# Kernel tuning notes

Measured on AMD Instinct MI355X. Metric: run time of the kernel, lower is better.

The kernel has to match this reference:

```python
import jax, jax.numpy as jnp
import numpy as np


def setup_inputs() -> dict:
    key = jax.random.key(0)
    ks = jax.random.split(key, 8)
    B, C, T, V = 64, 256, 64, 25
    h = 8
    x_cls = jax.random.normal(ks[0], (B, C, 1, V), dtype=jnp.float32)
    x_patch = jax.random.normal(ks[1], (B, C, T, V), dtype=jnp.float32)
    s = 0.02
    q_w = jax.random.normal(ks[2], (C, C), dtype=jnp.float32) * s
    k_w = jax.random.normal(ks[3], (C, C), dtype=jnp.float32) * s
    v_w = jax.random.normal(ks[4], (C, C), dtype=jnp.float32) * s
    temp = jnp.ones((h, 1), dtype=jnp.float32)
    proj_w = jax.random.normal(ks[5], (C, C), dtype=jnp.float32) * s
    proj_b = jnp.zeros((C,), dtype=jnp.float32)
    return {"x_cls": x_cls, "x_patch": x_patch, "q_w": q_w, "k_w": k_w,
            "v_w": v_w, "temp": temp, "proj_w": proj_w, "proj_b": proj_b}


def reference(x_cls, x_patch, q_w, k_w, v_w, temp, proj_w, proj_b):
    B, C, _, V = x_cls.shape
    T = x_patch.shape[2]
    h = temp.shape[0]
    hd = C // h
    # (B, C, 1, V) -> (B, V, C) token layout; patches -> (B, T*V, C)
    xc = jnp.transpose(x_cls.reshape(B, C, V), (0, 2, 1))
    xp = jnp.transpose(x_patch.reshape(B, C, T * V), (0, 2, 1))
    # nn.Linear: y = x @ W.T (no bias since qkv_bias=False)
    q = (xc @ q_w.T).reshape(B, V, h, hd).transpose(0, 2, 1, 3)        # (B,h,V,hd)
    k = (xp @ k_w.T).reshape(B, T * V, h, hd).transpose(0, 2, 1, 3)    # (B,h,TV,hd)
    v = (xp @ v_w.T).reshape(B, T * V, h, hd).transpose(0, 2, 1, 3)    # (B,h,TV,hd)
    # scores: (B,h,V,TV), scaled by 1/sqrt(hd) then per-head temperature
    scale = 1.0 / jnp.sqrt(jnp.asarray(hd, dtype=q.dtype))
    attn = jnp.einsum('bhqd,bhkd->bhqk', q, k) * scale
    attn = attn * temp[None, :, :, None]  # temp (h,1) -> broadcast (1,h,1,1)
    attn = jax.nn.softmax(attn, axis=-1)
    out = jnp.einsum('bhqk,bhkd->bhqd', attn, v)                       # (B,h,V,hd)
    out = out.transpose(0, 2, 1, 3).reshape(B, V, C)
    out = out @ proj_w.T + proj_b
    return jnp.transpose(out, (0, 2, 1)).reshape(B, C, 1, V)
```

## Files before the change

### kernel.cpp

```cpp
#include <hip/hip_runtime.h>

#define B_ 64
#define C_ 256
#define TV_ 1600
#define V_ 25
#define H_ 8

typedef __attribute__((ext_vector_type(2))) int   intx2;
typedef __attribute__((ext_vector_type(4))) int   intx4;
typedef __attribute__((ext_vector_type(4))) float floatx4;
typedef __attribute__((ext_vector_type(8))) short short8;

__device__ __forceinline__ unsigned short f2bf(float f) {
    union { float f; unsigned u; } c; c.f = f;
    unsigned u = c.u;
    u += 0x7fffu + ((u >> 16) & 1u);
    return (unsigned short)(u >> 16);
}
__device__ __forceinline__ float bf2f(unsigned short s) {
    union { unsigned u; float f; } c; c.u = ((unsigned)s) << 16;
    return c.f;
}
__device__ __forceinline__ int pk_bf2(float a, float b) {
    return (int)((unsigned)f2bf(a) | ((unsigned)f2bf(b) << 16));
}

__global__ __launch_bounds__(256) void kz_zero(float* __restrict__ zbase,
        const float* __restrict__ vw, const float* __restrict__ pw,
        unsigned short* __restrict__ VWB, unsigned short* __restrict__ PWB) {
    const int blk = blockIdx.x;
    if (blk < 528) {
        const int i = blk * 256 + threadIdx.x;
        ((floatx4*)zbase)[i] = (floatx4){0.f, 0.f, 0.f, 0.f};
    } else {
        const int g = (blk - 528) * 256 + threadIdx.x;
        const floatx4 v = ((const floatx4*)vw)[g];
        const floatx4 p = ((const floatx4*)pw)[g];
        ((intx2*)VWB)[g] = (intx2){pk_bf2(v[0], v[1]), pk_bf2(v[2], v[3])};
        ((intx2*)PWB)[g] = (intx2){pk_bf2(p[0], p[1]), pk_bf2(p[2], p[3])};
    }
}

__global__ __launch_bounds__(256) void k1_trans(const float* __restrict__ xp,
                                                unsigned short* __restrict__ XF) {
    __shared__ float xs[128 * 68];
    const int blk = blockIdx.x;
    const int b = blk / 25, nb = blk - b * 25;
    const int n0 = nb * 64;
    const int t = threadIdx.x;
    const int cl = t & 127, nh = (t >> 7) * 32;
    const int n = t & 63, cq = t >> 6;
    for (int p = 0; p < 2; p++) {
        const float* src = xp + ((size_t)(b * C_ + p * 128 + cl)) * TV_ + n0 + nh;
        floatx4 v[8];
        #pragma unroll
        for (int j = 0; j < 8; j++) v[j] = *(const floatx4*)(src + 4 * j);
        if (p) __syncthreads();
        #pragma unroll
        for (int j = 0; j < 8; j++) *(floatx4*)&xs[cl * 68 + nh + 4 * j] = v[j];
        __syncthreads();
        #pragma unroll
        for (int j4 = 0; j4 < 4; j4++) {
            const int cgl = cq * 4 + j4, c8 = cgl * 8;
            intx4 w;
            w[0] = pk_bf2(xs[(c8 + 0) * 68 + n], xs[(c8 + 1) * 68 + n]);
            w[1] = pk_bf2(xs[(c8 + 2) * 68 + n], xs[(c8 + 3) * 68 + n]);
            w[2] = pk_bf2(xs[(c8 + 4) * 68 + n], xs[(c8 + 5) * 68 + n]);
            w[3] = pk_bf2(xs[(c8 + 6) * 68 + n], xs[(c8 + 7) * 68 + n]);
            const size_t chunk = (size_t)(b * 50 + nb * 2 + (n >> 5)) * 1024
                               + (p * 16 + cgl) * 32 + (n & 31);
            *(intx4*)(XF + chunk * 8) = w;
        }
        if (!p) __syncthreads();
    }
}

__global__ __launch_bounds__(256) void k0_qtilde(const float* __restrict__ xcls,
        const float* __restrict__ qw, const float* __restrict__ kw,
        const float* __restrict__ temp, unsigned short* __restrict__ QT) {
    __shared__ float xq[25 * 260];
    __shared__ float qh[25 * 33];
    __shared__ float kws[32 * 264];
    const int blk = blockIdx.x;
    const int b = blk >> 3, h = blk & 7;
    const int t = threadIdx.x;
    {
        const float* src = xcls + ((size_t)(b * C_ + t)) * V_;
        #pragma unroll
        for (int q = 0; q < V_; q++) xq[q * 260 + t] = src[q];
    }
    {
        const int d = t >> 3, c0 = (t & 7) * 32;
        const float* src = kw + (size_t)(h * 32 + d) * C_ + c0;
        #pragma unroll
        for (int j4 = 0; j4 < 8; j4++)
            *(floatx4*)&kws[d * 264 + c0 + 4 * j4] = *(const floatx4*)(src + 4 * j4);
    }
    __syncthreads();
    for (int idx = t; idx < 800; idx += 256) {
        const int q = idx >> 5, d = idx & 31;
        const float* qwr = qw + (size_t)(h * 32 + d) * C_;
        float acc = 0.f;
        for (int c4 = 0; c4 < 64; c4++) {
            const floatx4 a = *(const floatx4*)(qwr + 4 * c4);
            const floatx4 x = *(const floatx4*)&xq[q * 260 + 4 * c4];
            acc += a[0] * x[0] + a[1] * x[1] + a[2] * x[2] + a[3] * x[3];
        }
        qh[q * 33 + d] = acc;
    }
    __syncthreads();
    const float scale = temp[h] * 0.17677669529663689f * 1.4426950408889634f;
    const int qp = t & 31, cg = t >> 5;
    const int c0 = cg * 32;
    if (qp < 25) {
        floatx4 a4[8];
        #pragma unroll
        for (int j = 0; j < 8; j++) a4[j] = (floatx4){0.f, 0.f, 0.f, 0.f};
        for (int d = 0; d < 32; d++) {
            const float a = qh[qp * 33 + d];
            #pragma unroll
            for (int j4 = 0; j4 < 8; j4++) {
                const floatx4 k4 = *(const floatx4*)&kws[d * 264 + c0 + 4 * j4];
                a4[j4][0] += a * k4[0]; a4[j4][1] += a * k4[1];
                a4[j4][2] += a * k4[2]; a4[j4][3] += a * k4[3];
            }
        }
        unsigned short* dst = QT + ((size_t)((b * H_ + h) * 25 + qp)) * C_ + c0;
        #pragma unroll
        for (int j8 = 0; j8 < 4; j8++) {
            intx4 w;
            w[0] = pk_bf2(scale * a4[j8 * 2][0],     scale * a4[j8 * 2][1]);
            w[1] = pk_bf2(scale * a4[j8 * 2][2],     scale * a4[j8 * 2][3]);
            w[2] = pk_bf2(scale * a4[j8 * 2 + 1][0], scale * a4[j8 * 2 + 1][1]);
            w[3] = pk_bf2(scale * a4[j8 * 2 + 1][2], scale * a4[j8 * 2 + 1][3]);
            *(intx4*)(dst + j8 * 8) = w;
        }
    }
}

__global__ __launch_bounds__(512, 2) void k2_attn(
        const unsigned short* __restrict__ XF, const unsigned short* __restrict__ QT,
        const unsigned short* __restrict__ VWB, float* __restrict__ OA,
        float* __restrict__ L) {
    __shared__ unsigned short Xs[8192];
    __shared__ unsigned short Ps[8][32 * 40];
    __shared__ unsigned short Vs[8][32 * 40];

    const int blk = blockIdx.x;
    const int b = blk & 63, s = blk >> 6;
    const int tid = threadIdx.x;
    const int h = tid >> 6;
    const int lane = tid & 63;
    const int quad = lane >> 4, l16 = lane & 15;

    short8 qf[2][8];
    {
        const unsigned short* qb = QT + (size_t)(b * H_ + h) * 25 * C_;
        #pragma unroll
        for (int mt = 0; mt < 2; mt++)
            #pragma unroll
            for (int ks = 0; ks < 8; ks++)
                qf[mt][ks] = *(const short8*)(qb + (mt * 16 + l16) * C_ + ks * 32 + quad * 8);
    }
    short8 vwf[2][8];
    #pragma unroll
    for (int dt = 0; dt < 2; dt++)
        #pragma unroll
        for (int ks = 0; ks < 8; ks++)
            vwf[dt][ks] = *(const short8*)(VWB + (size_t)(h * 32 + dt * 16 + l16) * C_ + ks * 32 + quad * 8);

    floatx4 oc[2][2];
    #pragma unroll
    for (int mt = 0; mt < 2; mt++)
        #pragma unroll
        for (int dt = 0; dt < 2; dt++) oc[mt][dt] = (floatx4){0.f, 0.f, 0.f, 0.f};
    float lsum[2][4];
    #pragma unroll
    for (int mt = 0; mt < 2; mt++)
        #pragma unroll
        for (int r = 0; r < 4; r++) lsum[mt][r] = 0.f;

    const unsigned short* xf_base = XF + (size_t)(b * 50 + s * 5) * 1024 * 8;
    intx4 px0 = *(const intx4*)(xf_base + (size_t)(tid * 2 + 0) * 8);
    intx4 px1 = *(const intx4*)(xf_base + (size_t)(tid * 2 + 1) * 8);

    for (int ti = 0; ti < 5; ti++) {
        *(intx4*)&Xs[(tid * 2 + 0) * 8] = px0;
        *(intx4*)&Xs[(tid * 2 + 1) * 8] = px1;
        __syncthreads();
        if (ti < 4) {
            const unsigned short* nxt = xf_base + (size_t)(ti + 1) * 1024 * 8;
            px0 = *(const intx4*)(nxt + (size_t)(tid * 2 + 0) * 8);
            px1 = *(const intx4*)(nxt + (size_t)(tid * 2 + 1) * 8);
        }
        floatx4 sc[2][2], va[2][2];
        #pragma unroll
        for (int i = 0; i < 2; i++)
            #pragma unroll
            for (int j = 0; j < 2; j++) {
                sc[i][j] = (floatx4){0.f, 0.f, 0.f, 0.f};
                va[i][j] = (floatx4){0.f, 0.f, 0.f, 0.f};
            }
        #pragma unroll
        for (int ks = 0; ks < 8; ks++) {
            const short8 xf0 = *(const short8*)&Xs[(((ks * 4 + quad) * 32) + l16) * 8];
            const short8 xf1 = *(const short8*)&Xs[(((ks * 4 + quad) * 32) + 16 + l16) * 8];
            sc[0][0] = __builtin_amdgcn_mfma_f32_16x16x32_bf16(qf[0][ks], xf0, sc[0][0], 0, 0, 0);
            sc[0][1] = __builtin_amdgcn_mfma_f32_16x16x32_bf16(qf[0][ks], xf1, sc[0][1], 0, 0, 0);
            sc[1][0] = __builtin_amdgcn_mfma_f32_16x16x32_bf16(qf[1][ks], xf0, sc[1][0], 0, 0, 0);
            sc[1][1] = __builtin_amdgcn_mfma_f32_16x16x32_bf16(qf[1][ks], xf1, sc[1][1], 0, 0, 0);
            va[0][0] = __builtin_amdgcn_mfma_f32_16x16x32_bf16(xf0, vwf[0][ks], va[0][0], 0, 0, 0);
            va[0][1] = __builtin_amdgcn_mfma_f32_16x16x32_bf16(xf0, vwf[1][ks], va[0][1], 0, 0, 0);
            va[1][0] = __builtin_amdgcn_mfma_f32_16x16x32_bf16(xf1, vwf[0][ks], va[1][0], 0, 0, 0);
            va[1][1] = __builtin_amdgcn_mfma_f32_16x16x32_bf16(xf1, vwf[1][ks], va[1][1], 0, 0, 0);
        }
        #pragma unroll
        for (int mt = 0; mt < 2; mt++)
            #pragma unroll
            for (int g = 0; g < 2; g++)
                #pragma unroll
                for (int r = 0; r < 4; r++) {
                    const float p = __builtin_amdgcn_exp2f(sc[mt][g][r]);
                    lsum[mt][r] += p;
                    Ps[h][(mt * 16 + quad * 4 + r) * 40 + g * 16 + l16] = f2bf(p);
                }
        #pragma unroll
        for (int g = 0; g < 2; g++)
            #pragma unroll
            for (int dt = 0; dt < 2; dt++)
                *(intx2*)&Vs[h][(dt * 16 + l16) * 40 + g * 16 + quad * 4] =
                    (intx2){pk_bf2(va[g][dt][0], va[g][dt][1]),
                            pk_bf2(va[g][dt][2], va[g][dt][3])};
        #pragma unroll
        for (int mt = 0; mt < 2; mt++) {
            const short8 pa = *(const short8*)&Ps[h][(mt * 16 + l16) * 40 + quad * 8];
            #pragma unroll
            for (int dt = 0; dt < 2; dt++) {
                const short8 vb = *(const short8*)&Vs[h][(dt * 16 + l16) * 40 + quad * 8];
                oc[mt][dt] = __builtin_amdgcn_mfma_f32_16x16x32_bf16(pa, vb, oc[mt][dt], 0, 0, 0);
            }
        }
        __syncthreads();
    }
    #pragma unroll
    for (int mt = 0; mt < 2; mt++)
        #pragma unroll
        for (int r = 0; r < 4; r++) {
            float v = lsum[mt][r];
            #pragma unroll
            for (int off = 1; off < 16; off <<= 1) v += __shfl_xor(v, off, 64);
            lsum[mt][r] = v;
        }
    const size_t bh = (size_t)(b * H_ + h);
    if (l16 == 0) {
        #pragma unroll
        for (int mt = 0; mt < 2; mt++)
            #pragma unroll
            for (int r = 0; r < 4; r++) {
                const int q = mt * 16 + quad * 4 + r;
                if (q < 25) atomicAdd(&L[bh * 32 + q], lsum[mt][r]);
            }
    }
    #pragma unroll
    for (int mt = 0; mt < 2; mt++)
        #pragma unroll
        for (int dt = 0; dt < 2; dt++)
            #pragma unroll
            for (int r = 0; r < 4; r++) {
                const int q = mt * 16 + quad * 4 + r;
                if (q < 25)
                    atomicAdd(&OA[bh * 1024 + q * 32 + dt * 16 + l16], oc[mt][dt][r]);
            }
}

__global__ __launch_bounds__(256) void k3_proj(const float* __restrict__ OA,
        const float* __restrict__ Lsum, const unsigned short* __restrict__ PWB,
        const float* __restrict__ pb, float* __restrict__ y) {
    __shared__ unsigned short OB[32 * 264];
    __shared__ float rl_s[256];
    const int blk = blockIdx.x;
    const int b = blk >> 1, i0 = (blk & 1) * 128;
    const int t = threadIdx.x;
    const int wv = t >> 6, lane = t & 63;
    const int quad = lane >> 4, l16 = lane & 15;
    {
        const int h = t >> 5, q = t & 31;
        const float lv = Lsum[(size_t)(b * H_ + h) * 32 + q];
        rl_s[t] = (q < 25) ? 1.0f / lv : 0.0f;
    }
    __syncthreads();
    for (int idx = t; idx < 8192; idx += 256) {
        const int q = idx >> 8, j = idx & 255;
        const int h2 = j >> 5, d = j & 31;
        const float val = (q < 25)
            ? OA[(size_t)(b * H_ + h2) * 1024 + q * 32 + d] * rl_s[h2 * 32 + q] : 0.f;
        OB[q * 264 + j] = f2bf(val);
    }
    __syncthreads();
    floatx4 oc[2][2];
    #pragma unroll
    for (int mt = 0; mt < 2; mt++)
        #pragma unroll
        for (int ntp = 0; ntp < 2; ntp++) oc[mt][ntp] = (floatx4){0.f, 0.f, 0.f, 0.f};
    #pragma unroll
    for (int ks = 0; ks < 8; ks++) {
        const short8 a0 = *(const short8*)&OB[l16 * 264 + ks * 32 + quad * 8];
        const short8 a1 = *(const short8*)&OB[(16 + l16) * 264 + ks * 32 + quad * 8];
        #pragma unroll
        for (int ntp = 0; ntp < 2; ntp++) {
            const int i = i0 + (wv * 2 + ntp) * 16 + l16;
            const short8 bv = *(const short8*)(PWB + (size_t)i * C_ + ks * 32 + quad * 8);
            oc[0][ntp] = __builtin_amdgcn_mfma_f32_16x16x32_bf16(a0, bv, oc[0][ntp], 0, 0, 0);
            oc[1][ntp] = __builtin_amdgcn_mfma_f32_16x16x32_bf16(a1, bv, oc[1][ntp], 0, 0, 0);
        }
    }
    #pragma unroll
    for (int ntp = 0; ntp < 2; ntp++) {
        const int i = i0 + (wv * 2 + ntp) * 16 + l16;
        const float bias = pb[i];
        #pragma unroll
        for (int mt = 0; mt < 2; mt++)
            #pragma unroll
            for (int r = 0; r < 4; r++) {
                const int q = mt * 16 + quad * 4 + r;
                if (q < 25) y[(size_t)b * 6400 + i * 25 + q] = oc[mt][ntp][r] + bias;
            }
    }
}

extern "C" void kernel_launch(void* const* d_in, const int* in_sizes, int n_in,
                              void* d_out, int out_size, void* d_ws, size_t ws_size,
                              hipStream_t stream) {
    const float* xcls = (const float*)d_in[0];
    const float* xp   = (const float*)d_in[1];
    const float* qw   = (const float*)d_in[2];
    const float* kw   = (const float*)d_in[3];
    const float* vw   = (const float*)d_in[4];
    const float* temp = (const float*)d_in[5];
    const float* pw   = (const float*)d_in[6];
    const float* pb   = (const float*)d_in[7];
    float* y = (float*)d_out;

    if (ws_size < (size_t)61415424) return;
    char* ws = (char*)d_ws;
    unsigned short* XF  = (unsigned short*)ws;
    unsigned short* QT  = (unsigned short*)(ws + 52428800);
    float*          OA  = (float*)(ws + 58990592);
    float*          L   = (float*)(ws + 61087744);
    unsigned short* VWB = (unsigned short*)(ws + 61153280);
    unsigned short* PWB = (unsigned short*)(ws + 61284352);

    hipLaunchKernelGGL(kz_zero,  dim3(592),  dim3(256), 0, stream, OA, vw, pw, VWB, PWB);
    hipLaunchKernelGGL(k1_trans, dim3(1600), dim3(256), 0, stream, xp, XF);
    hipLaunchKernelGGL(k0_qtilde,dim3(512),  dim3(256), 0, stream, xcls, qw, kw, temp, QT);
    hipLaunchKernelGGL(k2_attn,  dim3(640),  dim3(512), 0, stream, XF, QT, VWB, OA, L);
    hipLaunchKernelGGL(k3_proj,  dim3(128),  dim3(256), 0, stream, OA, L, PWB, pb, y);
}
```

Measured before the change: 299.6 us.

## Merge preprocessing kernels, double-buffer X tiles in attention, widen projection grid

Merges the zero/convert, transpose and q-tilde kernels into one launch that dispatches on block index, which removes two kernel launches and their serialization gaps. The q-tilde path now reads k_w straight from global memory instead of staging it in shared memory. The attention kernel double-buffers the X tile in LDS so the next tile is stored after compute, leaving one barrier per iteration. The projection kernel uses twice as many blocks, each computing half as many output columns, to raise parallelism at the cost of redundant OB staging.

Result: no change. 296.6 us (-1.0%).

```diff
diff --git a/kernel.cpp b/kernel.cpp
--- a/kernel.cpp
+++ b/kernel.cpp
@@ -25,115 +25,110 @@
     return (int)((unsigned)f2bf(a) | ((unsigned)f2bf(b) << 16));
 }
 
-__global__ __launch_bounds__(256) void kz_zero(float* __restrict__ zbase,
+__global__ __launch_bounds__(256) void k_pre(
+        const float* __restrict__ xp, unsigned short* __restrict__ XF,
+        const float* __restrict__ xcls, const float* __restrict__ qw,
+        const float* __restrict__ kw, const float* __restrict__ temp,
+        unsigned short* __restrict__ QT,
+        float* __restrict__ zbase,
         const float* __restrict__ vw, const float* __restrict__ pw,
         unsigned short* __restrict__ VWB, unsigned short* __restrict__ PWB) {
+    __shared__ float smem[128 * 68];
     const int blk = blockIdx.x;
-    if (blk < 528) {
-        const int i = blk * 256 + threadIdx.x;
-        ((floatx4*)zbase)[i] = (floatx4){0.f, 0.f, 0.f, 0.f};
+    const int t = threadIdx.x;
+
+    if (blk < 1600) {
+        float* xs = smem;
+        const int b = blk / 25, nb = blk - b * 25;
+        const int n0 = nb * 64;
+        const int cl = t & 127, nh = (t >> 7) * 32;
+        const int n = t & 63, cq = t >> 6;
+        for (int p = 0; p < 2; p++) {
+            const float* src = xp + ((size_t)(b * C_ + p * 128 + cl)) * TV_ + n0 + nh;
+            floatx4 v[8];
+            #pragma unroll
+            for (int j = 0; j < 8; j++) v[j] = *(const floatx4*)(src + 4 * j);
+            if (p) __syncthreads();
+            #pragma unroll
+            for (int j = 0; j < 8; j++) *(floatx4*)&xs[cl * 68 + nh + 4 * j] = v[j];
+            __syncthreads();
+            #pragma unroll
+            for (int j4 = 0; j4 < 4; j4++) {
+                const int cgl = cq * 4 + j4, c8 = cgl * 8;
+                intx4 w;
+                w[0] = pk_bf2(xs[(c8 + 0) * 68 + n], xs[(c8 + 1) * 68 + n]);
+                w[1] = pk_bf2(xs[(c8 + 2) * 68 + n], xs[(c8 + 3) * 68 + n]);
+                w[2] = pk_bf2(xs[(c8 + 4) * 68 + n], xs[(c8 + 5) * 68 + n]);
+                w[3] = pk_bf2(xs[(c8 + 6) * 68 + n], xs[(c8 + 7) * 68 + n]);
+                const size_t chunk = (size_t)(b * 50 + nb * 2 + (n >> 5)) * 1024
+                                   + (p * 16 + cgl) * 32 + (n & 31);
+                *(intx4*)(XF + chunk * 8) = w;
+            }
+            if (!p) __syncthreads();
+        }
+    } else if (blk < 2112) {
+        float* xq = smem;
+        float* qh = smem + 6500;
+        const int blk2 = blk - 1600;
+        const int b = blk2 >> 3, h = blk2 & 7;
+        {
+            const float* src = xcls + ((size_t)(b * C_ + t)) * V_;
+            #pragma unroll
+            for (int q = 0; q < V_; q++) xq[q * 260 + t] = src[q];
+        }
+        __syncthreads();
+        for (int idx = t; idx < 800; idx += 256) {
+            const int q = idx >> 5, d = idx & 31;
+            const float* qwr = qw + (size_t)(h * 32 + d) * C_;
+            float acc = 0.f;
+            for (int c4 = 0; c4 < 64; c4++) {
+                const floatx4 a = *(const floatx4*)(qwr + 4 * c4);
+                const floatx4 x = *(const floatx4*)&xq[q * 260 + 4 * c4];
+                acc += a[0] * x[0] + a[1] * x[1] + a[2] * x[2] + a[3] * x[3];
+            }
+            qh[q * 33 + d] = acc;
+        }
+        __syncthreads();
+        const float scale = temp[h] * 0.17677669529663689f * 1.4426950408889634f;
+        const int qp = t & 31, cg = t >> 5;
+        const int c0 = cg * 32;
+        if (qp < 25) {
+            floatx4 a4[8];
+            #pragma unroll
+            for (int j = 0; j < 8; j++) a4[j] = (floatx4){0.f, 0.f, 0.f, 0.f};
+            const float* kwb = kw + (size_t)(h * 32) * C_ + c0;
+            for (int d = 0; d < 32; d++) {
+                const float a = qh[qp * 33 + d];
+                const float* kr = kwb + (size_t)d * C_;
+                #pragma unroll
+                for (int j4 = 0; j4 < 8; j4++) {
+                    const floatx4 k4 = *(const floatx4*)(kr + 4 * j4);
+                    a4[j4][0] += a * k4[0]; a4[j4][1] += a * k4[1];
+                    a4[j4][2] += a * k4[2]; a4[j4][3] += a * k4[3];
+                }
+            }
+            unsigned short* dst = QT + ((size_t)((b * H_ + h) * 25 + qp)) * C_ + c0;
+            #pragma unroll
+            for (int j8 = 0; j8 < 4; j8++) {
+                intx4 w;
+                w[0] = pk_bf2(scale * a4[j8 * 2][0],     scale * a4[j8 * 2][1]);
+                w[1] = pk_bf2(scale * a4[j8 * 2][2],     scale * a4[j8 * 2][3]);
+                w[2] = pk_bf2(scale * a4[j8 * 2 + 1][0], scale * a4[j8 * 2 + 1][1]);
+                w[3] = pk_bf2(scale * a4[j8 * 2 + 1][2], scale * a4[j8 * 2 + 1][3]);
+                *(intx4*)(dst + j8 * 8) = w;
+            }
+        }
     } else {
-        const int g = (blk - 528) * 256 + threadIdx.x;
-        const floatx4 v = ((const floatx4*)vw)[g];
-        const floatx4 p = ((const floatx4*)pw)[g];
-        ((intx2*)VWB)[g] = (intx2){pk_bf2(v[0], v[1]), pk_bf2(v[2], v[3])};
-        ((intx2*)PWB)[g] = (intx2){pk_bf2(p[0], p[1]), pk_bf2(p[2], p[3])};
-    }
-}
-
-__global__ __launch_bounds__(256) void k1_trans(const float* __restrict__ xp,
-                                                unsigned short* __restrict__ XF) {
-    __shared__ float xs[128 * 68];
-    const int blk = blockIdx.x;
-    const int b = blk / 25, nb = blk - b * 25;
-    const int n0 = nb * 64;
-    const int t = threadIdx.x;
-    const int cl = t & 127, nh = (t >> 7) * 32;
-    const int n = t & 63, cq = t >> 6;
-    for (int p = 0; p < 2; p++) {
-        const float* src = xp + ((size_t)(b * C_ + p * 128 + cl)) * TV_ + n0 + nh;
-        floatx4 v[8];
-        #pragma unroll
-        for (int j = 0; j < 8; j++) v[j] = *(const floatx4*)(src + 4 * j);
-        if (p) __syncthreads();
-        #pragma unroll
-        for (int j = 0; j < 8; j++) *(floatx4*)&xs[cl * 68 + nh + 4 * j] = v[j];
-        __syncthreads();
-        #pragma unroll
-        for (int j4 = 0; j4 < 4; j4++) {
-            const int cgl = cq * 4 + j4, c8 = cgl * 8;
-            intx4 w;
-            w[0] = pk_bf2(xs[(c8 + 0) * 68 + n], xs[(c8 + 1) * 68 + n]);
-            w[1] = pk_bf2(xs[(c8 + 2) * 68 + n], xs[(c8 + 3) * 68 + n]);
-            w[2] = pk_bf2(xs[(c8 + 4) * 68 + n], xs[(c8 + 5) * 68 + n]);
-            w[3] = pk_bf2(xs[(c8 + 6) * 68 + n], xs[(c8 + 7) * 68 + n]);
-            const size_t chunk = (size_t)(b * 50 + nb * 2 + (n >> 5)) * 1024
-                               + (p * 16 + cgl) * 32 + (n & 31);
-            *(intx4*)(XF + chunk * 8) = w;
-        }
-        if (!p) __syncthreads();
-    }
-}
-
-__global__ __launch_bounds__(256) void k0_qtilde(const float* __restrict__ xcls,
-        const float* __restrict__ qw, const float* __restrict__ kw,
-        const float* __restrict__ temp, unsigned short* __restrict__ QT) {
-    __shared__ float xq[25 * 260];
-    __shared__ float qh[25 * 33];
-    __shared__ float kws[32 * 264];
-    const int blk = blockIdx.x;
-    const int b = blk >> 3, h = blk & 7;
-    const int t = threadIdx.x;
-    {
-        const float* src = xcls + ((size_t)(b * C_ + t)) * V_;
-        #pragma unroll
-        for (int q = 0; q < V_; q++) xq[q * 260 + t] = src[q];
-    }
-    {
-        const int d = t >> 3, c0 = (t & 7) * 32;
-        const float* src = kw + (size_t)(h * 32 + d) * C_ + c0;
-        #pragma unroll
-        for (int j4 = 0; j4 < 8; j4++)
-            *(floatx4*)&kws[d * 264 + c0 + 4 * j4] = *(const floatx4*)(src + 4 * j4);
-    }
-    __syncthreads();
-    for (int idx = t; idx < 800; idx += 256) {
-        const int q = idx >> 5, d = idx & 31;
-        const float* qwr = qw + (size_t)(h * 32 + d) * C_;
-        float acc = 0.f;
-        for (int c4 = 0; c4 < 64; c4++) {
-            const floatx4 a = *(const floatx4*)(qwr + 4 * c4);
-            const floatx4 x = *(const floatx4*)&xq[q * 260 + 4 * c4];
-            acc += a[0] * x[0] + a[1] * x[1] + a[2] * x[2] + a[3] * x[3];
-        }
-        qh[q * 33 + d] = acc;
-    }
-    __syncthreads();
-    const float scale = temp[h] * 0.17677669529663689f * 1.4426950408889634f;
-    const int qp = t & 31, cg = t >> 5;
-    const int c0 = cg * 32;
-    if (qp < 25) {
-        floatx4 a4[8];
-        #pragma unroll
-        for (int j = 0; j < 8; j++) a4[j] = (floatx4){0.f, 0.f, 0.f, 0.f};
-        for (int d = 0; d < 32; d++) {
-            const float a = qh[qp * 33 + d];
-            #pragma unroll
-            for (int j4 = 0; j4 < 8; j4++) {
-                const floatx4 k4 = *(const floatx4*)&kws[d * 264 + c0 + 4 * j4];
-                a4[j4][0] += a * k4[0]; a4[j4][1] += a * k4[1];
-                a4[j4][2] += a * k4[2]; a4[j4][3] += a * k4[3];
-            }
-        }
-        unsigned short* dst = QT + ((size_t)((b * H_ + h) * 25 + qp)) * C_ + c0;
-        #pragma unroll
-        for (int j8 = 0; j8 < 4; j8++) {
-            intx4 w;
-            w[0] = pk_bf2(scale * a4[j8 * 2][0],     scale * a4[j8 * 2][1]);
-            w[1] = pk_bf2(scale * a4[j8 * 2][2],     scale * a4[j8 * 2][3]);
-            w[2] = pk_bf2(scale * a4[j8 * 2 + 1][0], scale * a4[j8 * 2 + 1][1]);
-            w[3] = pk_bf2(scale * a4[j8 * 2 + 1][2], scale * a4[j8 * 2 + 1][3]);
-            *(intx4*)(dst + j8 * 8) = w;
+        const int blk3 = blk - 2112;
+        if (blk3 < 528) {
+            const int i = blk3 * 256 + t;
+            ((floatx4*)zbase)[i] = (floatx4){0.f, 0.f, 0.f, 0.f};
+        } else {
+            const int g = (blk3 - 528) * 256 + t;
+            const floatx4 v = ((const floatx4*)vw)[g];
+            const floatx4 p = ((const floatx4*)pw)[g];
+            ((intx2*)VWB)[g] = (intx2){pk_bf2(v[0], v[1]), pk_bf2(v[2], v[3])};
+            ((intx2*)PWB)[g] = (intx2){pk_bf2(p[0], p[1]), pk_bf2(p[2], p[3])};
         }
     }
 }
@@ -142,7 +137,7 @@
         const unsigned short* __restrict__ XF, const unsigned short* __restrict__ QT,
         const unsigned short* __restrict__ VWB, float* __restrict__ OA,
         float* __restrict__ L) {
-    __shared__ unsigned short Xs[8192];
+    __shared__ unsigned short Xs[2][8192];
     __shared__ unsigned short Ps[8][32 * 40];
     __shared__ unsigned short Vs[8][32 * 40];
 
@@ -183,16 +178,18 @@
     const unsigned short* xf_base = XF + (size_t)(b * 50 + s * 5) * 1024 * 8;
     intx4 px0 = *(const intx4*)(xf_base + (size_t)(tid * 2 + 0) * 8);
     intx4 px1 = *(const intx4*)(xf_base + (size_t)(tid * 2 + 1) * 8);
+    *(intx4*)&Xs[0][(tid * 2 + 0) * 8] = px0;
+    *(intx4*)&Xs[0][(tid * 2 + 1) * 8] = px1;
+    __syncthreads();
 
     for (int ti = 0; ti < 5; ti++) {
-        *(intx4*)&Xs[(tid * 2 + 0) * 8] = px0;
-        *(intx4*)&Xs[(tid * 2 + 1) * 8] = px1;
-        __syncthreads();
+        const int cur = ti & 1;
         if (ti < 4) {
             const unsigned short* nxt = xf_base + (size_t)(ti + 1) * 1024 * 8;
             px0 = *(const intx4*)(nxt + (size_t)(tid * 2 + 0) * 8);
             px1 = *(const intx4*)(nxt + (size_t)(tid * 2 + 1) * 8);
         }
+        const unsigned short* xsc = Xs[cur];
         floatx4 sc[2][2], va[2][2];
         #pragma unroll
         for (int i = 0; i < 2; i++)
@@ -203,8 +200,8 @@
             }
         #pragma unroll
         for (int ks = 0; ks < 8; ks++) {
-            const short8 xf0 = *(const short8*)&Xs[(((ks * 4 + quad) * 32) + l16) * 8];
-            const short8 xf1 = *(const short8*)&Xs[(((ks * 4 + quad) * 32) + 16 + l16) * 8];
+            const short8 xf0 = *(const short8*)&xsc[(((ks * 4 + quad) * 32) + l16) * 8];
+            const short8 xf1 = *(const short8*)&xsc[(((ks * 4 + quad) * 32) + 16 + l16) * 8];
             sc[0][0] = __builtin_amdgcn_mfma_f32_16x16x32_bf16(qf[0][ks], xf0, sc[0][0], 0, 0, 0);
             sc[0][1] = __builtin_amdgcn_mfma_f32_16x16x32_bf16(qf[0][ks], xf1, sc[0][1], 0, 0, 0);
             sc[1][0] = __builtin_amdgcn_mfma_f32_16x16x32_bf16(qf[1][ks], xf0, sc[1][0], 0, 0, 0);
@@ -240,6 +237,10 @@
                 oc[mt][dt] = __builtin_amdgcn_mfma_f32_16x16x32_bf16(pa, vb, oc[mt][dt], 0, 0, 0);
             }
         }
+        if (ti < 4) {
+            *(intx4*)&Xs[cur ^ 1][(tid * 2 + 0) * 8] = px0;
+            *(intx4*)&Xs[cur ^ 1][(tid * 2 + 1) * 8] = px1;
+        }
         __syncthreads();
     }
     #pragma unroll
@@ -279,7 +280,7 @@
     __shared__ unsigned short OB[32 * 264];
     __shared__ float rl_s[256];
     const int blk = blockIdx.x;
-    const int b = blk >> 1, i0 = (blk & 1) * 128;
+    const int b = blk >> 2, i0 = (blk & 3) * 64;
     const int t = threadIdx.x;
     const int wv = t >> 6, lane = t & 63;
     const int quad = lane >> 4, l16 = lane & 15;
@@ -297,35 +298,26 @@
         OB[q * 264 + j] = f2bf(val);
     }
     __syncthreads();
-    floatx4 oc[2][2];
-    #pragma unroll
-    for (int mt = 0; mt < 2; mt++)
-        #pragma unroll
-        for (int ntp = 0; ntp < 2; ntp++) oc[mt][ntp] = (floatx4){0.f, 0.f, 0.f, 0.f};
+    floatx4 oc[2];
+    oc[0] = (floatx4){0.f, 0.f, 0.f, 0.f};
+    oc[1] = (floatx4){0.f, 0.f, 0.f, 0.f};
+    const int i = i0 + wv * 16 + l16;
     #pragma unroll
     for (int ks = 0; ks < 8; ks++) {
         const short8 a0 = *(const short8*)&OB[l16 * 264 + ks * 32 + quad * 8];
         const short8 a1 = *(const short8*)&OB[(16 + l16) * 264 + ks * 32 + quad * 8];
-        #pragma unroll
-        for (int ntp = 0; ntp < 2; ntp++) {
-            const int i = i0 + (wv * 2 + ntp) * 16 + l16;
-            const short8 bv = *(const short8*)(PWB + (size_t)i * C_ + ks * 32 + quad * 8);
-            oc[0][ntp] = __builtin_amdgcn_mfma_f32_16x16x32_bf16(a0, bv, oc[0][ntp], 0, 0, 0);
-            oc[1][ntp] = __builtin_amdgcn_mfma_f32_16x16x32_bf16(a1, bv, oc[1][ntp], 0, 0, 0);
-        }
-    }
-    #pragma unroll
-    for (int ntp = 0; ntp < 2; ntp++) {
-        const int i = i0 + (wv * 2 + ntp) * 16 + l16;
-        const float bias = pb[i];
-        #pragma unroll
-        for (int mt = 0; mt < 2; mt++)
-            #pragma unroll
-            for (int r = 0; r < 4; r++) {
-                const int q = mt * 16 + quad * 4 + r;
-                if (q < 25) y[(size_t)b * 6400 + i * 25 + q] = oc[mt][ntp][r] + bias;
-            }
-    }
+        const short8 bv = *(const short8*)(PWB + (size_t)i * C_ + ks * 32 + quad * 8);
+        oc[0] = __builtin_amdgcn_mfma_f32_16x16x32_bf16(a0, bv, oc[0], 0, 0, 0);
+        oc[1] = __builtin_amdgcn_mfma_f32_16x16x32_bf16(a1, bv, oc[1], 0, 0, 0);
+    }
+    const float bias = pb[i];
+    #pragma unroll
+    for (int mt = 0; mt < 2; mt++)
+        #pragma unroll
+        for (int r = 0; r < 4; r++) {
+            const int q = mt * 16 + quad * 4 + r;
+            if (q < 25) y[(size_t)b * 6400 + i * 25 + q] = oc[mt][r] + bias;
+        }
 }
 
 extern "C" void kernel_launch(void* const* d_in, const int* in_sizes, int n_in,
@@ -350,9 +342,8 @@
     unsigned short* VWB = (unsigned short*)(ws + 61153280);
     unsigned short* PWB = (unsigned short*)(ws + 61284352);
 
-    hipLaunchKernelGGL(kz_zero,  dim3(592),  dim3(256), 0, stream, OA, vw, pw, VWB, PWB);
-    hipLaunchKernelGGL(k1_trans, dim3(1600), dim3(256), 0, stream, xp, XF);
-    hipLaunchKernelGGL(k0_qtilde,dim3(512),  dim3(256), 0, stream, xcls, qw, kw, temp, QT);
-    hipLaunchKernelGGL(k2_attn,  dim3(640),  dim3(512), 0, stream, XF, QT, VWB, OA, L);
-    hipLaunchKernelGGL(k3_proj,  dim3(128),  dim3(256), 0, stream, OA, L, PWB, pb, y);
-}
+    hipLaunchKernelGGL(k_pre,   dim3(2704), dim3(256), 0, stream,
+                       xp, XF, xcls, qw, kw, temp, QT, OA, vw, pw, VWB, PWB);
+    hipLaunchKernelGGL(k2_attn, dim3(640),  dim3(512), 0, stream, XF, QT, VWB, OA, L);
+    hipLaunchKernelGGL(k3_proj, dim3(256),  dim3(256), 0, stream, OA, L, PWB, pb, y);
+}
```
